# Optimization experiments

Hardware: AMD Instinct MI355X
Metric: run time of the kernel (lower is better)

Reference implementation:

```python
import jax, jax.numpy as jnp
import numpy as np

B, S, H = 1024, 16, 1024
N = 16384          # retrieved neighbors per user
L = 128            # num_labels


def setup_inputs() -> dict:
    key = jax.random.key(0)
    ks = jax.random.split(key, 6)
    features = jax.random.normal(ks[0], (B, S, H), dtype=jnp.float32)
    sims = jax.random.uniform(ks[1], (B, N), dtype=jnp.float32)
    labels = jax.random.randint(ks[2], (B, N), 0, L, dtype=jnp.int32)
    dense_w = jax.random.normal(ks[3], (H, H + L), dtype=jnp.float32) * 0.02
    dense_b = jnp.zeros((H,), dtype=jnp.float32)
    out_w = jax.random.normal(ks[4], (L, H), dtype=jnp.float32) * 0.02
    out_b = jnp.zeros((L,), dtype=jnp.float32)
    return {
        "features": features,
        "user_texts_similarities": sims,
        "user_texts_labels": labels,
        "dense_w": dense_w,
        "dense_b": dense_b,
        "out_w": out_w,
        "out_b": out_b,
    }


def _aggregate_labels(sims, labels):
    # mean over N of one_hot(labels) * sims  ->  scatter-add then divide.
    b, n = sims.shape
    agg = jnp.zeros((b, L), dtype=sims.dtype)
    rows = jnp.arange(b, dtype=jnp.int32)[:, None]  # [B,1] broadcast against [B,N]
    agg = agg.at[rows, labels].add(sims)
    return agg / n  # [B, L]


def reference(features, user_texts_similarities, user_texts_labels,
              dense_w, dense_b, out_w, out_b):
    # top_k=None, normalize_weights=False, feature_normalization='none', eval (dropout=id)
    agg = _aggregate_labels(user_texts_similarities, user_texts_labels)  # [B, L]
    cls = features[:, 0, :]                                              # [B, H]
    x = jnp.concatenate((cls, agg), axis=1)                              # [B, H+L]
    x = jnp.tanh(x @ dense_w.T + dense_b)                                # [B, H]
    return x @ out_w.T + out_b                                           # [B, L]
```

## Files before the change

kernel.cpp:

```cpp
#include <hip/hip_runtime.h>

#define B_DIM 1024
#define S_DIM 16
#define H_DIM 1024
#define N_DIM 16384
#define L_DIM 128
#define KX    (H_DIM + L_DIM)

typedef __bf16 bf16_8 __attribute__((ext_vector_type(8)));
typedef float  f32x4  __attribute__((ext_vector_type(4)));

__device__ __forceinline__ unsigned short f2bf(float f) {
    unsigned int u = __float_as_uint(f);
    u += 0x7fffu + ((u >> 16) & 1u);
    return (unsigned short)(u >> 16);
}

#define GLD16(gp, lp)                                                          \
    __builtin_amdgcn_global_load_lds(                                          \
        (const __attribute__((address_space(1))) void*)(gp),                   \
        (__attribute__((address_space(3))) void*)(lp), 16, 0, 0)

__global__ __launch_bounds__(256) void k_agg(
    const float* __restrict__ feats,
    const float* __restrict__ sims,
    const int*   __restrict__ labels,
    unsigned short* __restrict__ xin)
{
    __shared__ float binsT[L_DIM][64];
    const int b = blockIdx.x;
    const int t = threadIdx.x;
    const int c = t & 63;

    float* flat = (float*)binsT;
    #pragma unroll
    for (int i = 0; i < L_DIM * 64 / 256; ++i) flat[t + i * 256] = 0.f;
    __syncthreads();

    const float4* s4 = (const float4*)(sims   + (size_t)b * N_DIM);
    const int4*   l4 = (const int4*)  (labels + (size_t)b * N_DIM);
    #pragma unroll 4
    for (int v = t; v < N_DIM / 4; v += 256) {
        float4 s  = s4[v];
        int4   li = l4[v];
        atomicAdd(&binsT[li.x][c], s.x);
        atomicAdd(&binsT[li.y][c], s.y);
        atomicAdd(&binsT[li.z][c], s.z);
        atomicAdd(&binsT[li.w][c], s.w);
    }
    __syncthreads();

    unsigned short* xrow = xin + (size_t)b * KX;
    const float4* c4 = (const float4*)(feats + (size_t)b * (S_DIM * H_DIM));
    float4 cv = c4[t];
    ushort4 p;
    p.x = f2bf(cv.x); p.y = f2bf(cv.y); p.z = f2bf(cv.z); p.w = f2bf(cv.w);
    *(ushort4*)(xrow + t * 4) = p;

    if (t < L_DIM) {
        float s = 0.f;
        #pragma unroll
        for (int i = 0; i < 64; ++i) s += binsT[t][(i + t) & 63];
        xrow[H_DIM + t] = f2bf(s * (1.0f / N_DIM));
    }
}

__global__ __launch_bounds__(256) void k_cvt(
    const float* __restrict__ w1, const float* __restrict__ w2,
    unsigned short* __restrict__ o1, unsigned short* __restrict__ o2,
    int n1v, int n2v)
{
    int idx = blockIdx.x * 256 + threadIdx.x;
    int stride = gridDim.x * 256;
    for (int i = idx; i < n1v + n2v; i += stride) {
        const float4* src; unsigned short* dst; int j;
        if (i < n1v) { src = (const float4*)w1; dst = o1; j = i; }
        else         { src = (const float4*)w2; dst = o2; j = i - n1v; }
        float4 v = src[j];
        ushort4 p;
        p.x = f2bf(v.x); p.y = f2bf(v.y); p.z = f2bf(v.z); p.w = f2bf(v.w);
        *(ushort4*)(dst + j * 4) = p;
    }
}

template <int EPI>
__global__ __launch_bounds__(256) void k_gemm_bt(
    const unsigned short* __restrict__ A,
    const unsigned short* __restrict__ Bm,
    const float* __restrict__ bias,
    void* __restrict__ Cout,
    int M, int N, int K, int ldc)
{
    __shared__ __align__(16) unsigned short smA[3][64 * 64];
    __shared__ __align__(16) unsigned short smB[3][32 * 64];

    const int t    = threadIdx.x;
    const int lane = t & 63;
    const int w    = t >> 6;
    const int wm   = w >> 1, wn = w & 1;
    const int m0   = blockIdx.y * 64;
    const int n0   = blockIdx.x * 32;
    const int lr   = lane & 15;
    const int hi   = lane >> 4;

    int srcA[2];
    #pragma unroll
    for (int j = 0; j < 2; ++j) {
        int li  = t + j * 256;
        int row = li >> 3;
        int g   = (li & 7) ^ (row & 7);
        srcA[j] = row * K + g * 8;
    }
    const int rowB = t >> 3;
    const int gB   = (t & 7) ^ (rowB & 7);
    const int srcB = rowB * K + gB * 8;

    const size_t aBase = (size_t)m0 * K;
    const size_t bBase = (size_t)n0 * K;

    const int nt = K >> 6;
    f32x4 acc[2] = {};

#define STAGE(buf, k0_)                                                        \
    do {                                                                       \
        GLD16(Bm + bBase + (size_t)(srcB + (k0_)), &smB[buf][t * 8]);          \
        _Pragma("unroll")                                                      \
        for (int j = 0; j < 2; ++j) {                                          \
            int li = t + j * 256;                                              \
            GLD16(A + aBase + (size_t)(srcA[j] + (k0_)), &smA[buf][li * 8]);   \
        }                                                                      \
    } while (0)

    STAGE(0, 0);
    if (nt > 1) STAGE(1, 64);

    int cur = 0;
    for (int ti = 0; ti < nt; ++ti) {
        int b2 = cur + 2; if (b2 >= 3) b2 -= 3;
        if (ti + 2 < nt) {
            STAGE(b2, (ti + 2) << 6);
            asm volatile("s_waitcnt vmcnt(6)" ::: "memory");
        } else if (ti + 1 < nt) {
            asm volatile("s_waitcnt vmcnt(3)" ::: "memory");
        } else {
            asm volatile("s_waitcnt vmcnt(0)" ::: "memory");
        }
        __builtin_amdgcn_s_barrier();
        asm volatile("" ::: "memory");

        const unsigned short* As = smA[cur];
        const unsigned short* Bs = smB[cur];
        #pragma unroll
        for (int ks = 0; ks < 2; ++ks) {
            const int gl = ks * 4 + hi;
            const int ga = (gl ^ (lr & 7)) * 8;
            bf16_8 a0 = *(const bf16_8*)(As + (wm * 32 +      lr) * 64 + ga);
            bf16_8 a1 = *(const bf16_8*)(As + (wm * 32 + 16 + lr) * 64 + ga);
            bf16_8 b0 = *(const bf16_8*)(Bs + (wn * 16 +      lr) * 64 + ga);
            acc[0] = __builtin_amdgcn_mfma_f32_16x16x32_bf16(a0, b0, acc[0], 0, 0, 0);
            acc[1] = __builtin_amdgcn_mfma_f32_16x16x32_bf16(a1, b0, acc[1], 0, 0, 0);
        }

        asm volatile("" ::: "memory");
        __builtin_amdgcn_s_barrier();
        cur = cur + 1; if (cur >= 3) cur = 0;
    }

    const int rbase = m0 + wm * 32 + hi * 4;
    const int col   = n0 + wn * 16 + lr;
    const float bv  = bias[col];
    #pragma unroll
    for (int i = 0; i < 2; ++i) {
        #pragma unroll
        for (int r = 0; r < 4; ++r) {
            int row = rbase + i * 16 + r;
            float v = acc[i][r] + bv;
            if (EPI == 0) {
                v = tanhf(v);
                ((unsigned short*)Cout)[(size_t)row * ldc + col] = f2bf(v);
            } else {
                ((float*)Cout)[(size_t)row * ldc + col] = v;
            }
        }
    }
#undef STAGE
}

extern "C" void kernel_launch(void* const* d_in, const int* in_sizes, int n_in,
                              void* d_out, int out_size, void* d_ws, size_t ws_size,
                              hipStream_t stream) {
    const float* feats   = (const float*)d_in[0];
    const float* sims    = (const float*)d_in[1];
    const int*   labels  = (const int*)  d_in[2];
    const float* dense_w = (const float*)d_in[3];
    const float* dense_b = (const float*)d_in[4];
    const float* out_w   = (const float*)d_in[5];
    const float* out_b   = (const float*)d_in[6];
    float* out = (float*)d_out;

    unsigned short* xin  = (unsigned short*)d_ws;
    unsigned short* wd   = xin  + (size_t)B_DIM * KX;
    unsigned short* wo   = wd   + (size_t)H_DIM * KX;
    unsigned short* xmid = wo   + (size_t)L_DIM * H_DIM;

    k_agg<<<B_DIM, 256, 0, stream>>>(feats, sims, labels, xin);

    int n1v = (H_DIM * KX) / 4;
    int n2v = (L_DIM * H_DIM) / 4;
    k_cvt<<<512, 256, 0, stream>>>(dense_w, out_w, wd, wo, n1v, n2v);

    dim3 g1(H_DIM / 32, B_DIM / 64);
    k_gemm_bt<0><<<g1, 256, 0, stream>>>(xin, wd, dense_b, (void*)xmid,
                                         B_DIM, H_DIM, KX, H_DIM);

    dim3 g2(L_DIM / 32, B_DIM / 64);
    k_gemm_bt<1><<<g2, 256, 0, stream>>>(xmid, wo, out_b, (void*)out,
                                         B_DIM, L_DIM, H_DIM, L_DIM);
}
```

Before: 254.8 us.

## Replace atomic label histogram with private per-lane bins; enlarge GEMM tiles

```diff
diff --git a/kernel.cpp b/kernel.cpp
--- a/kernel.cpp
+++ b/kernel.cpp
@@ -21,48 +21,89 @@
         (const __attribute__((address_space(1))) void*)(gp),                   \
         (__attribute__((address_space(3))) void*)(lp), 16, 0, 0)
 
-__global__ __launch_bounds__(256) void k_agg(
+__global__ __launch_bounds__(64) void k_agg(
     const float* __restrict__ feats,
     const float* __restrict__ sims,
     const int*   __restrict__ labels,
     unsigned short* __restrict__ xin)
 {
-    __shared__ float binsT[L_DIM][64];
-    const int b = blockIdx.x;
-    const int t = threadIdx.x;
-    const int c = t & 63;
-
-    float* flat = (float*)binsT;
-    #pragma unroll
-    for (int i = 0; i < L_DIM * 64 / 256; ++i) flat[t + i * 256] = 0.f;
+    __shared__ float bins[129 * 64];
+    const int bb = blockIdx.x;
+    const int t  = threadIdx.x;
+
+    #pragma unroll
+    for (int i = 0; i < 129; ++i) bins[i * 64 + t] = 0.f;
     __syncthreads();
 
-    const float4* s4 = (const float4*)(sims   + (size_t)b * N_DIM);
-    const int4*   l4 = (const int4*)  (labels + (size_t)b * N_DIM);
-    #pragma unroll 4
-    for (int v = t; v < N_DIM / 4; v += 256) {
-        float4 s  = s4[v];
-        int4   li = l4[v];
-        atomicAdd(&binsT[li.x][c], s.x);
-        atomicAdd(&binsT[li.y][c], s.y);
-        atomicAdd(&binsT[li.z][c], s.z);
-        atomicAdd(&binsT[li.w][c], s.w);
+    const float4* s4 = (const float4*)(sims   + (size_t)bb * N_DIM);
+    const int4*   l4 = (const int4*)  (labels + (size_t)bb * N_DIM);
+
+    float4 fs[2][4];
+    int4   fl[2][4];
+
+#define LOADB(slot, bt)                                                        \
+    do {                                                                       \
+        _Pragma("unroll")                                                      \
+        for (int q = 0; q < 4; ++q) {                                          \
+            fs[slot][q] = s4[((bt) * 4 + q) * 64 + t];                         \
+            fl[slot][q] = l4[((bt) * 4 + q) * 64 + t];                         \
+        }                                                                      \
+    } while (0)
+
+#define UPD4(sv, lv)                                                           \
+    do {                                                                       \
+        int   l0 = (lv).x, l1 = (lv).y, l2 = (lv).z, l3 = (lv).w;              \
+        float v0 = (sv).x, v1 = (sv).y, v2 = (sv).z, v3 = (sv).w;              \
+        if (l1 == l0) { v0 += v1; v1 = 0.f; l1 = 128; }                        \
+        if (l2 == l0) { v0 += v2; v2 = 0.f; l2 = 128; }                        \
+        if (l3 == l0) { v0 += v3; v3 = 0.f; l3 = 128; }                        \
+        if (l2 == l1) { v1 += v2; v2 = 0.f; l2 = 128; }                        \
+        if (l3 == l1) { v1 += v3; v3 = 0.f; l3 = 128; }                        \
+        if (l3 == l2) { v2 += v3; v3 = 0.f; l3 = 128; }                        \
+        float* p0 = &bins[l0 * 64 + t];                                        \
+        float* p1 = &bins[l1 * 64 + t];                                        \
+        float* p2 = &bins[l2 * 64 + t];                                        \
+        float* p3 = &bins[l3 * 64 + t];                                        \
+        float r0 = *p0, r1 = *p1, r2 = *p2, r3 = *p3;                          \
+        *p0 = r0 + v0; *p1 = r1 + v1; *p2 = r2 + v2; *p3 = r3 + v3;            \
+    } while (0)
+
+    LOADB(0, 0);
+    LOADB(1, 1);
+    #pragma unroll
+    for (int bt = 0; bt < 16; ++bt) {
+        const int sl = bt & 1;
+        #pragma unroll
+        for (int q = 0; q < 4; ++q) UPD4(fs[sl][q], fl[sl][q]);
+        if (bt + 2 < 16) LOADB(sl, bt + 2);
     }
     __syncthreads();
 
-    unsigned short* xrow = xin + (size_t)b * KX;
-    const float4* c4 = (const float4*)(feats + (size_t)b * (S_DIM * H_DIM));
-    float4 cv = c4[t];
-    ushort4 p;
-    p.x = f2bf(cv.x); p.y = f2bf(cv.y); p.z = f2bf(cv.z); p.w = f2bf(cv.w);
-    *(ushort4*)(xrow + t * 4) = p;
-
-    if (t < L_DIM) {
-        float s = 0.f;
-        #pragma unroll
-        for (int i = 0; i < 64; ++i) s += binsT[t][(i + t) & 63];
-        xrow[H_DIM + t] = f2bf(s * (1.0f / N_DIM));
-    }
+    unsigned short* xrow = xin + (size_t)bb * KX;
+    const float4* c4 = (const float4*)(feats + (size_t)bb * (S_DIM * H_DIM));
+    #pragma unroll
+    for (int i = 0; i < 4; ++i) {
+        float4 cv = c4[t + i * 64];
+        ushort4 p;
+        p.x = f2bf(cv.x); p.y = f2bf(cv.y); p.z = f2bf(cv.z); p.w = f2bf(cv.w);
+        *(ushort4*)(xrow + (t + i * 64) * 4) = p;
+    }
+
+    #pragma unroll
+    for (int pb = 0; pb < 2; ++pb) {
+        const int l = pb * 64 + t;
+        float a0 = 0.f, a1 = 0.f, a2 = 0.f, a3 = 0.f;
+        #pragma unroll
+        for (int i = 0; i < 64; i += 4) {
+            a0 += bins[l * 64 + ((t + i)     & 63)];
+            a1 += bins[l * 64 + ((t + i + 1) & 63)];
+            a2 += bins[l * 64 + ((t + i + 2) & 63)];
+            a3 += bins[l * 64 + ((t + i + 3) & 63)];
+        }
+        xrow[H_DIM + l] = f2bf((a0 + a1 + a2 + a3) * (1.0f / N_DIM));
+    }
+#undef LOADB
+#undef UPD4
 }
 
 __global__ __launch_bounds__(256) void k_cvt(
@@ -84,51 +125,56 @@
 }
 
 template <int EPI>
-__global__ __launch_bounds__(256) void k_gemm_bt(
+__global__ __launch_bounds__(256) void k_gemm(
     const unsigned short* __restrict__ A,
     const unsigned short* __restrict__ Bm,
     const float* __restrict__ bias,
     void* __restrict__ Cout,
     int M, int N, int K, int ldc)
 {
-    __shared__ __align__(16) unsigned short smA[3][64 * 64];
-    __shared__ __align__(16) unsigned short smB[3][32 * 64];
+    __shared__ __align__(16) unsigned short smA[3][128 * 64];
+    __shared__ __align__(16) unsigned short smB[3][64 * 64];
 
     const int t    = threadIdx.x;
     const int lane = t & 63;
     const int w    = t >> 6;
-    const int wm   = w >> 1, wn = w & 1;
-    const int m0   = blockIdx.y * 64;
-    const int n0   = blockIdx.x * 32;
+    const int m0   = blockIdx.y * 128;
+    const int n0   = blockIdx.x * 64;
     const int lr   = lane & 15;
     const int hi   = lane >> 4;
-
-    int srcA[2];
+    const int sw   = lr & 7;
+
+    int srcA[4], srcB[2];
+    #pragma unroll
+    for (int j = 0; j < 4; ++j) {
+        int idx = t + j * 256;
+        int row = idx >> 3;
+        int g   = (idx & 7) ^ (row & 7);
+        srcA[j] = row * K + g * 8;
+    }
     #pragma unroll
     for (int j = 0; j < 2; ++j) {
-        int li  = t + j * 256;
-        int row = li >> 3;
-        int g   = (li & 7) ^ (row & 7);
-        srcA[j] = row * K + g * 8;
-    }
-    const int rowB = t >> 3;
-    const int gB   = (t & 7) ^ (rowB & 7);
-    const int srcB = rowB * K + gB * 8;
-
+        int idx = t + j * 256;
+        int row = idx >> 3;
+        int g   = (idx & 7) ^ (row & 7);
+        srcB[j] = row * K + g * 8;
+    }
     const size_t aBase = (size_t)m0 * K;
     const size_t bBase = (size_t)n0 * K;
 
     const int nt = K >> 6;
-    f32x4 acc[2] = {};
+    f32x4 acc[2][4] = {};
 
 #define STAGE(buf, k0_)                                                        \
     do {                                                                       \
-        GLD16(Bm + bBase + (size_t)(srcB + (k0_)), &smB[buf][t * 8]);          \
         _Pragma("unroll")                                                      \
-        for (int j = 0; j < 2; ++j) {                                          \
-            int li = t + j * 256;                                              \
-            GLD16(A + aBase + (size_t)(srcA[j] + (k0_)), &smA[buf][li * 8]);   \
-        }                                                                      \
+        for (int j = 0; j < 4; ++j)                                            \
+            GLD16(A + aBase + (size_t)(srcA[j] + (k0_)),                       \
+                  &smA[buf][(t + j * 256) * 8]);                               \
+        _Pragma("unroll")                                                      \
+        for (int j = 0; j < 2; ++j)                                            \
+            GLD16(Bm + bBase + (size_t)(srcB[j] + (k0_)),                      \
+                  &smB[buf][(t + j * 256) * 8]);                               \
     } while (0)
 
     STAGE(0, 0);
@@ -139,9 +185,9 @@
         int b2 = cur + 2; if (b2 >= 3) b2 -= 3;
         if (ti + 2 < nt) {
             STAGE(b2, (ti + 2) << 6);
+            asm volatile("s_waitcnt vmcnt(12)" ::: "memory");
+        } else if (ti + 1 < nt) {
             asm volatile("s_waitcnt vmcnt(6)" ::: "memory");
-        } else if (ti + 1 < nt) {
-            asm volatile("s_waitcnt vmcnt(3)" ::: "memory");
         } else {
             asm volatile("s_waitcnt vmcnt(0)" ::: "memory");
         }
@@ -152,13 +198,21 @@
         const unsigned short* Bs = smB[cur];
         #pragma unroll
         for (int ks = 0; ks < 2; ++ks) {
-            const int gl = ks * 4 + hi;
-            const int ga = (gl ^ (lr & 7)) * 8;
-            bf16_8 a0 = *(const bf16_8*)(As + (wm * 32 +      lr) * 64 + ga);
-            bf16_8 a1 = *(const bf16_8*)(As + (wm * 32 + 16 + lr) * 64 + ga);
-            bf16_8 b0 = *(const bf16_8*)(Bs + (wn * 16 +      lr) * 64 + ga);
-            acc[0] = __builtin_amdgcn_mfma_f32_16x16x32_bf16(a0, b0, acc[0], 0, 0, 0);
-            acc[1] = __builtin_amdgcn_mfma_f32_16x16x32_bf16(a1, b0, acc[1], 0, 0, 0);
+            const int ga = ((ks * 4 + hi) ^ sw) * 8;
+            bf16_8 a0 = *(const bf16_8*)(As + (w * 32 +      lr) * 64 + ga);
+            bf16_8 a1 = *(const bf16_8*)(As + (w * 32 + 16 + lr) * 64 + ga);
+            bf16_8 b0 = *(const bf16_8*)(Bs + (      lr) * 64 + ga);
+            bf16_8 b1 = *(const bf16_8*)(Bs + (16  + lr) * 64 + ga);
+            bf16_8 b2v = *(const bf16_8*)(Bs + (32 + lr) * 64 + ga);
+            bf16_8 b3 = *(const bf16_8*)(Bs + (48  + lr) * 64 + ga);
+            acc[0][0] = __builtin_amdgcn_mfma_f32_16x16x32_bf16(a0, b0,  acc[0][0], 0, 0, 0);
+            acc[1][0] = __builtin_amdgcn_mfma_f32_16x16x32_bf16(a1, b0,  acc[1][0], 0, 0, 0);
+            acc[0][1] = __builtin_amdgcn_mfma_f32_16x16x32_bf16(a0, b1,  acc[0][1], 0, 0, 0);
+            acc[1][1] = __builtin_amdgcn_mfma_f32_16x16x32_bf16(a1, b1,  acc[1][1], 0, 0, 0);
+            acc[0][2] = __builtin_amdgcn_mfma_f32_16x16x32_bf16(a0, b2v, acc[0][2], 0, 0, 0);
+            acc[1][2] = __builtin_amdgcn_mfma_f32_16x16x32_bf16(a1, b2v, acc[1][2], 0, 0, 0);
+            acc[0][3] = __builtin_amdgcn_mfma_f32_16x16x32_bf16(a0, b3,  acc[0][3], 0, 0, 0);
+            acc[1][3] = __builtin_amdgcn_mfma_f32_16x16x32_bf16(a1, b3,  acc[1][3], 0, 0, 0);
         }
 
         asm volatile("" ::: "memory");
@@ -166,20 +220,24 @@
         cur = cur + 1; if (cur >= 3) cur = 0;
     }
 
-    const int rbase = m0 + wm * 32 + hi * 4;
-    const int col   = n0 + wn * 16 + lr;
-    const float bv  = bias[col];
+    const int rbase = m0 + w * 32 + hi * 4;
+    const int cbase = n0 + lr;
     #pragma unroll
     for (int i = 0; i < 2; ++i) {
         #pragma unroll
-        for (int r = 0; r < 4; ++r) {
-            int row = rbase + i * 16 + r;
-            float v = acc[i][r] + bv;
-            if (EPI == 0) {
-                v = tanhf(v);
-                ((unsigned short*)Cout)[(size_t)row * ldc + col] = f2bf(v);
-            } else {
-                ((float*)Cout)[(size_t)row * ldc + col] = v;
+        for (int j = 0; j < 4; ++j) {
+            int col = cbase + j * 16;
+            float bv = bias[col];
+            #pragma unroll
+            for (int r = 0; r < 4; ++r) {
+                int row = rbase + i * 16 + r;
+                float v = acc[i][j][r] + bv;
+                if (EPI == 0) {
+                    v = tanhf(v);
+                    ((unsigned short*)Cout)[(size_t)row * ldc + col] = f2bf(v);
+                } else {
+                    ((float*)Cout)[(size_t)row * ldc + col] = v;
+                }
             }
         }
     }
@@ -203,17 +261,17 @@
     unsigned short* wo   = wd   + (size_t)H_DIM * KX;
     unsigned short* xmid = wo   + (size_t)L_DIM * H_DIM;
 
-    k_agg<<<B_DIM, 256, 0, stream>>>(feats, sims, labels, xin);
+    k_agg<<<B_DIM, 64, 0, stream>>>(feats, sims, labels, xin);
 
     int n1v = (H_DIM * KX) / 4;
     int n2v = (L_DIM * H_DIM) / 4;
     k_cvt<<<512, 256, 0, stream>>>(dense_w, out_w, wd, wo, n1v, n2v);
 
-    dim3 g1(H_DIM / 32, B_DIM / 64);
-    k_gemm_bt<0><<<g1, 256, 0, stream>>>(xin, wd, dense_b, (void*)xmid,
-                                         B_DIM, H_DIM, KX, H_DIM);
-
-    dim3 g2(L_DIM / 32, B_DIM / 64);
-    k_gemm_bt<1><<<g2, 256, 0, stream>>>(xmid, wo, out_b, (void*)out,
-                                         B_DIM, L_DIM, H_DIM, L_DIM);
-}
+    dim3 g1(H_DIM / 64, B_DIM / 128);
+    k_gemm<0><<<g1, 256, 0, stream>>>(xin, wd, dense_b, (void*)xmid,
+                                      B_DIM, H_DIM, KX, H_DIM);
+
+    dim3 g2(L_DIM / 64, B_DIM / 128);
+    k_gemm<1><<<g2, 256, 0, stream>>>(xmid, wo, out_b, (void*)out,
+                                      B_DIM, L_DIM, H_DIM, L_DIM);
+}
```

Result: faster. 224.9 us (-11.7%).
